# Kernel tuning notes

Measured on AMD Instinct MI355X. Metric: run time of the kernel, lower is better.

Reference implementation:

```python
import jax, jax.numpy as jnp
import numpy as np

B, S, TRG, SRC2 = 64, 2048, 512, 1024  # batch, src_len, trg_hidden, 2*src_hidden


def setup_inputs() -> dict:
    key = jax.random.key(0)
    ks = jax.random.split(key, 9)
    return {
        "dehy": jax.random.normal(ks[0], (B, TRG), dtype=jnp.float32),
        "enhy": jax.random.normal(ks[1], (B, S, SRC2), dtype=jnp.float32),
        "past_attn": jax.random.uniform(ks[2], (B, S), dtype=jnp.float32),
        "src_mask": jax.random.randint(ks[3], (B, S), 0, 2, dtype=jnp.int32),
        # parameters (torch Linear: y = x @ W.T + b)
        "W_en": jax.random.normal(ks[4], (TRG, SRC2), dtype=jnp.float32) * 0.02,
        "b_en": jnp.zeros((TRG,), dtype=jnp.float32),
        "W_de": jax.random.normal(ks[5], (TRG, TRG), dtype=jnp.float32) * 0.02,
        "w_cv": jax.random.normal(ks[6], (TRG,), dtype=jnp.float32) * 0.02,   # attn_cv_in: Linear(1, trg)
        "w_warp": jax.random.normal(ks[7], (TRG,), dtype=jnp.float32) * 0.02, # attn_warp_in: Linear(trg, 1)
    }


def reference(dehy, enhy, past_attn, src_mask, W_en, b_en, W_de, w_cv, w_warp):
    # luong_concat score with 'asee' coverage term
    # attn_agg: [B, S, TRG]
    attn_agg = (
        jnp.einsum("bsd,hd->bsh", enhy, W_en) + b_en
        + (dehy @ W_de.T)[:, None, :]
        + past_attn[..., None] * w_cv
    )
    attn_agg = jnp.tanh(attn_agg)
    attn_ee = jnp.einsum("bsh,h->bs", attn_agg, w_warp)  # [B, S]
    # masked_fill(|mask| == 0, -1e20)
    attn_ee = jnp.where(jnp.abs(src_mask) == 0, jnp.float32(-1e20), attn_ee)
    attn = jax.nn.softmax(attn_ee, axis=1)
    c_encoder = jnp.einsum("bs,bsd->bd", attn, enhy)  # [B, SRC2]
    return (c_encoder, attn, attn_ee)
```

## Files before the change

kernel.cpp:

```cpp
#include <hip/hip_runtime.h>
#include <hip/hip_bf16.h>

#define B_   64
#define S_   2048
#define TRG_ 512
#define K_   1024

typedef short short8 __attribute__((ext_vector_type(8)));
typedef short short4v __attribute__((ext_vector_type(4)));
typedef float f32x4  __attribute__((ext_vector_type(4)));
typedef unsigned short us4 __attribute__((ext_vector_type(4)));

__device__ __forceinline__ unsigned short f2bf(float f) {
    union { float f; unsigned int u; } v; v.f = f;
    unsigned int u = v.u;
    unsigned int r = (u + 0x7fffu + ((u >> 16) & 1u)) >> 16;
    return (unsigned short)r;
}

__device__ __forceinline__ short4v cvt4(f32x4 a) {
    union { __hip_bfloat162 h[2]; short4v v; } u;
    u.h[0] = __float22bfloat162_rn(float2{a[0], a[1]});
    u.h[1] = __float22bfloat162_rn(float2{a[2], a[3]});
    return u.v;
}

__global__ void wen_convert_kernel(const float* __restrict__ Wen,
                                   unsigned short* __restrict__ Wbf) {
    int idx = blockIdx.x * 256 + threadIdx.x;
    float4 f = ((const float4*)Wen)[idx];
    us4 o = { f2bf(f.x), f2bf(f.y), f2bf(f.z), f2bf(f.w) };
    ((us4*)Wbf)[idx] = o;
}

__global__ void deproj_kernel(const float* __restrict__ dehy,
                              const float* __restrict__ Wde,
                              const float* __restrict__ ben,
                              float* __restrict__ dp) {
    int b = blockIdx.x >> 1;
    int h = ((blockIdx.x & 1) << 8) + threadIdx.x;
    const float4* dv = (const float4*)(dehy + (size_t)b * TRG_);
    const float4* wv = (const float4*)(Wde + (size_t)h * TRG_);
    float s = ben[h];
    #pragma unroll 4
    for (int t = 0; t < TRG_ / 4; ++t) {
        float4 a = dv[t], w = wv[t];
        s += a.x * w.x + a.y * w.y + a.z * w.z + a.w * w.w;
    }
    dp[b * TRG_ + h] = s;
}

__global__ __launch_bounds__(512, 4) void score_kernel(
    const float* __restrict__ enhy,
    const unsigned short* __restrict__ Wbf,
    const float* __restrict__ dp,
    const float* __restrict__ past_attn,
    const int* __restrict__ src_mask,
    const float* __restrict__ w_cv,
    const float* __restrict__ w_warp,
    float* __restrict__ out_ee)
{
    __shared__ unsigned short Bbuf[2][512 * 32];
    __shared__ unsigned short Abuf[2][64 * 32];
    __shared__ float red[8][64];

    const int tid  = threadIdx.x;
    const int lane = tid & 63;
    const int w    = tid >> 6;
    const int lj   = lane & 15;
    const int lg   = lane >> 4;
    const int m0   = blockIdx.x * 64;
    const int b    = m0 >> 11;

    const int kx = ((lg ^ ((lj >> 1) & 3)) << 4);

    f32x4 acc[4][4];
    const f32x4 fz = {0.f, 0.f, 0.f, 0.f};
    #pragma unroll
    for (int i = 0; i < 4; ++i)
        #pragma unroll
        for (int j = 0; j < 4; ++j) acc[i][j] = fz;

    const int arow = tid >> 3;
    const int akq  = tid & 7;
    const float* aSrc = enhy + (size_t)(m0 + arow) * K_ + (akq << 2);
    const int aDstByte = arow * 64 + (((akq >> 1) ^ ((arow >> 1) & 3)) << 4) + ((akq & 1) << 3);

    const int brow0 = tid >> 2;
    const int bkc0  = tid & 3;
    const unsigned short* bSrc0 = Wbf + (size_t)brow0 * K_ + ((bkc0 ^ ((brow0 >> 1) & 3)) << 3);
    const int bDst0 = w * 1024;

#define LOADA(R, kt) { R = __builtin_nontemporal_load((const f32x4*)(aSrc + ((kt) << 5))); }
#define WRITEA(sel, R) { \
    *(short4v*)((char*)&Abuf[0][0] + (sel) * 4096 + aDstByte) = cvt4(R); }
#define STAGEB(sel, kt) { \
    _Pragma("unroll") \
    for (int j_ = 0; j_ < 4; ++j_) { \
        __builtin_amdgcn_global_load_lds( \
            (const __attribute__((address_space(1))) void*)(bSrc0 + (size_t)j_ * 128 * K_ + ((kt) << 5)), \
            (__attribute__((address_space(3))) void*)((char*)&Bbuf[0][0] + (sel) * 32768 + bDst0 + j_ * 8192), \
            16, 0, 0); \
    } }

    auto compute = [&](int sel) {
        const char* Bbase = (const char*)&Bbuf[0][0] + sel * 32768;
        const char* Abase = (const char*)&Abuf[0][0] + sel * 4096;
        short8 bfr[4];
        #pragma unroll
        for (int fn = 0; fn < 4; ++fn) {
            int r = (w << 6) + (fn << 4) + lj;
            bfr[fn] = *(const short8*)(Bbase + r * 64 + kx);
        }
        #pragma unroll
        for (int fm = 0; fm < 4; ++fm) {
            int rA = (fm << 4) + lj;
            short8 af = *(const short8*)(Abase + rA * 64 + kx);
            #pragma unroll
            for (int fn = 0; fn < 4; ++fn)
                acc[fm][fn] = __builtin_amdgcn_mfma_f32_16x16x32_bf16(af, bfr[fn], acc[fm][fn], 0, 0, 0);
        }
    };

    f32x4 a_c, a_n;
    LOADA(a_c, 0);
    STAGEB(0, 0);
    WRITEA(0, a_c);
    __syncthreads();

    #pragma unroll 2
    for (int kt = 0; kt < 32; ++kt) {
        const int cur = kt & 1, nxt = cur ^ 1;
        if (kt < 31) {
            STAGEB(nxt, kt + 1);
            LOADA(a_n, kt + 1);
        }
        compute(cur);
        if (kt < 31) WRITEA(nxt, a_n);
        __syncthreads();
    }

#undef LOADA
#undef WRITEA
#undef STAGEB

    float dep4[4], wcv4[4], wwp4[4];
    #pragma unroll
    for (int fn = 0; fn < 4; ++fn) {
        int h = (w << 6) + (fn << 4) + lj;
        dep4[fn] = dp[b * TRG_ + h];
        wcv4[fn] = w_cv[h];
        wwp4[fn] = w_warp[h];
    }
    #pragma unroll
    for (int fm = 0; fm < 4; ++fm) {
        #pragma unroll
        for (int reg = 0; reg < 4; ++reg) {
            int row = (fm << 4) + (lg << 2) + reg;
            float pa = past_attn[m0 + row];
            float p = 0.f;
            #pragma unroll
            for (int fn = 0; fn < 4; ++fn) {
                float v = acc[fm][fn][reg] + dep4[fn] + pa * wcv4[fn];
                float e = __expf(2.f * v);
                float t = 1.f - 2.f * __builtin_amdgcn_rcpf(e + 1.f);
                p += t * wwp4[fn];
            }
            p += __shfl_xor(p, 1);
            p += __shfl_xor(p, 2);
            p += __shfl_xor(p, 4);
            p += __shfl_xor(p, 8);
            if (lj == 0) red[w][row] = p;
        }
    }
    __syncthreads();
    if (tid < 64) {
        float ee = 0.f;
        #pragma unroll
        for (int ww = 0; ww < 8; ++ww) ee += red[ww][tid];
        int msk = src_mask[m0 + tid];
        if (msk == 0) ee = -1e20f;
        out_ee[m0 + tid] = ee;
    }
}

__global__ void softmax_kernel(const float* __restrict__ ee, float* __restrict__ attn) {
    int b = blockIdx.x, tid = threadIdx.x;
    const float* row = ee + (size_t)b * S_;
    float v[8]; float mx = -3.0e38f;
    #pragma unroll
    for (int i = 0; i < 8; ++i) { v[i] = row[tid + (i << 8)]; mx = fmaxf(mx, v[i]); }
    #pragma unroll
    for (int off = 32; off > 0; off >>= 1) mx = fmaxf(mx, __shfl_xor(mx, off));
    __shared__ float sred[4];
    int w = tid >> 6, lane = tid & 63;
    if (lane == 0) sred[w] = mx;
    __syncthreads();
    mx = fmaxf(fmaxf(sred[0], sred[1]), fmaxf(sred[2], sred[3]));
    float sum = 0.f;
    #pragma unroll
    for (int i = 0; i < 8; ++i) { v[i] = __expf(v[i] - mx); sum += v[i]; }
    #pragma unroll
    for (int off = 32; off > 0; off >>= 1) sum += __shfl_xor(sum, off);
    __syncthreads();
    if (lane == 0) sred[w] = sum;
    __syncthreads();
    sum = sred[0] + sred[1] + sred[2] + sred[3];
    float inv = 1.f / sum;
    float* orow = attn + (size_t)b * S_;
    #pragma unroll
    for (int i = 0; i < 8; ++i) orow[tid + (i << 8)] = v[i] * inv;
}

__global__ void ctx_partial_kernel(const float* __restrict__ attn,
                                   const float* __restrict__ enhy,
                                   float* __restrict__ part) {
    int bx = blockIdx.x;
    int b = bx >> 5, sc = bx & 31;
    int tid = threadIdx.x;
    const float4* e4 = (const float4*)(enhy + ((size_t)b * S_ + sc * 64) * K_);
    const float* ar = attn + (size_t)b * S_ + sc * 64;
    float4 acc = {0.f, 0.f, 0.f, 0.f};
    #pragma unroll 8
    for (int s = 0; s < 64; ++s) {
        float a = ar[s];
        float4 ev = e4[(size_t)s * 256 + tid];
        acc.x += a * ev.x; acc.y += a * ev.y; acc.z += a * ev.z; acc.w += a * ev.w;
    }
    ((float4*)part)[(size_t)(sc * 64 + b) * 256 + tid] = acc;
}

__global__ void ctx_reduce_kernel(const float* __restrict__ part, float* __restrict__ outc) {
    int idx = blockIdx.x * 256 + threadIdx.x;
    int b = idx >> 10, d = idx & 1023;
    float s = 0.f;
    #pragma unroll
    for (int sc = 0; sc < 32; ++sc) s += part[(size_t)((sc << 6) + b) * 1024 + d];
    outc[idx] = s;
}

extern "C" void kernel_launch(void* const* d_in, const int* in_sizes, int n_in,
                              void* d_out, int out_size, void* d_ws, size_t ws_size,
                              hipStream_t stream) {
    (void)in_sizes; (void)n_in; (void)out_size; (void)ws_size;

    const float* dehy = (const float*)d_in[0];
    const float* enhy = (const float*)d_in[1];
    const float* past = (const float*)d_in[2];
    const int*   mask = (const int*)d_in[3];
    const float* Wen  = (const float*)d_in[4];
    const float* ben  = (const float*)d_in[5];
    const float* Wde  = (const float*)d_in[6];
    const float* wcv  = (const float*)d_in[7];
    const float* wwp  = (const float*)d_in[8];

    float* out      = (float*)d_out;
    float* out_c    = out;
    float* out_attn = out + 65536;
    float* out_ee   = out + 65536 + 131072;

    char* ws = (char*)d_ws;
    unsigned short* Wbf = (unsigned short*)ws;
    float* dp   = (float*)(ws + (1 << 20));
    float* part = (float*)(ws + (1 << 20) + (1 << 17));

    wen_convert_kernel<<<512, 256, 0, stream>>>(Wen, Wbf);
    deproj_kernel<<<128, 256, 0, stream>>>(dehy, Wde, ben, dp);
    score_kernel<<<2048, 512, 0, stream>>>(enhy, Wbf, dp, past, mask, wcv, wwp, out_ee);
    softmax_kernel<<<64, 256, 0, stream>>>(out_ee, out_attn);
    ctx_partial_kernel<<<2048, 256, 0, stream>>>(out_attn, enhy, part);
    ctx_reduce_kernel<<<256, 256, 0, stream>>>(part, out_c);
}
```

Before: 376.8 us.

## Load W fragments directly into registers and deepen A prefetch to two stages

```diff
diff --git a/kernel.cpp b/kernel.cpp
--- a/kernel.cpp
+++ b/kernel.cpp
@@ -60,7 +60,6 @@
     const float* __restrict__ w_warp,
     float* __restrict__ out_ee)
 {
-    __shared__ unsigned short Bbuf[2][512 * 32];
     __shared__ unsigned short Abuf[2][64 * 32];
     __shared__ float red[8][64];
 
@@ -86,63 +85,56 @@
     const float* aSrc = enhy + (size_t)(m0 + arow) * K_ + (akq << 2);
     const int aDstByte = arow * 64 + (((akq >> 1) ^ ((arow >> 1) & 3)) << 4) + ((akq & 1) << 3);
 
-    const int brow0 = tid >> 2;
-    const int bkc0  = tid & 3;
-    const unsigned short* bSrc0 = Wbf + (size_t)brow0 * K_ + ((bkc0 ^ ((brow0 >> 1) & 3)) << 3);
-    const int bDst0 = w * 1024;
+    const unsigned short* bRow = Wbf + (size_t)((w << 6) + lj) * K_ + (lg << 3);
 
 #define LOADA(R, kt) { R = __builtin_nontemporal_load((const f32x4*)(aSrc + ((kt) << 5))); }
 #define WRITEA(sel, R) { \
     *(short4v*)((char*)&Abuf[0][0] + (sel) * 4096 + aDstByte) = cvt4(R); }
-#define STAGEB(sel, kt) { \
+#define LOADB(B0, B1, B2, B3, kt) { const int ko_ = (kt) << 5; \
+    B0 = *(const short8*)(bRow + (size_t)(0 * 16) * K_ + ko_); \
+    B1 = *(const short8*)(bRow + (size_t)(1 * 16) * K_ + ko_); \
+    B2 = *(const short8*)(bRow + (size_t)(2 * 16) * K_ + ko_); \
+    B3 = *(const short8*)(bRow + (size_t)(3 * 16) * K_ + ko_); }
+#define COMPUTE(sel, B0, B1, B2, B3) { \
+    const char* Abase = (const char*)&Abuf[0][0] + (sel) * 4096; \
     _Pragma("unroll") \
-    for (int j_ = 0; j_ < 4; ++j_) { \
-        __builtin_amdgcn_global_load_lds( \
-            (const __attribute__((address_space(1))) void*)(bSrc0 + (size_t)j_ * 128 * K_ + ((kt) << 5)), \
-            (__attribute__((address_space(3))) void*)((char*)&Bbuf[0][0] + (sel) * 32768 + bDst0 + j_ * 8192), \
-            16, 0, 0); \
+    for (int fm = 0; fm < 4; ++fm) { \
+        short8 af = *(const short8*)(Abase + ((fm << 4) + lj) * 64 + kx); \
+        acc[fm][0] = __builtin_amdgcn_mfma_f32_16x16x32_bf16(af, B0, acc[fm][0], 0, 0, 0); \
+        acc[fm][1] = __builtin_amdgcn_mfma_f32_16x16x32_bf16(af, B1, acc[fm][1], 0, 0, 0); \
+        acc[fm][2] = __builtin_amdgcn_mfma_f32_16x16x32_bf16(af, B2, acc[fm][2], 0, 0, 0); \
+        acc[fm][3] = __builtin_amdgcn_mfma_f32_16x16x32_bf16(af, B3, acc[fm][3], 0, 0, 0); \
     } }
 
-    auto compute = [&](int sel) {
-        const char* Bbase = (const char*)&Bbuf[0][0] + sel * 32768;
-        const char* Abase = (const char*)&Abuf[0][0] + sel * 4096;
-        short8 bfr[4];
-        #pragma unroll
-        for (int fn = 0; fn < 4; ++fn) {
-            int r = (w << 6) + (fn << 4) + lj;
-            bfr[fn] = *(const short8*)(Bbase + r * 64 + kx);
-        }
-        #pragma unroll
-        for (int fm = 0; fm < 4; ++fm) {
-            int rA = (fm << 4) + lj;
-            short8 af = *(const short8*)(Abase + rA * 64 + kx);
-            #pragma unroll
-            for (int fn = 0; fn < 4; ++fn)
-                acc[fm][fn] = __builtin_amdgcn_mfma_f32_16x16x32_bf16(af, bfr[fn], acc[fm][fn], 0, 0, 0);
-        }
-    };
-
+#define STEP(kt, BC0,BC1,BC2,BC3, BN0,BN1,BN2,BN3, AW, AL, DOB, DOA, DOW) { \
+    if (DOB) LOADB(BN0, BN1, BN2, BN3, (kt) + 1) \
+    if (DOA) LOADA(AL, (kt) + 2) \
+    COMPUTE((kt) & 1, BC0, BC1, BC2, BC3) \
+    if (DOW) WRITEA(((kt) & 1) ^ 1, AW) \
+    __syncthreads(); \
+}
+
+    short8 bA0, bA1, bA2, bA3, bB0, bB1, bB2, bB3;
     f32x4 a_c, a_n;
+
     LOADA(a_c, 0);
-    STAGEB(0, 0);
+    LOADB(bA0, bA1, bA2, bA3, 0)
     WRITEA(0, a_c);
-    __syncthreads();
-
-    #pragma unroll 2
-    for (int kt = 0; kt < 32; ++kt) {
-        const int cur = kt & 1, nxt = cur ^ 1;
-        if (kt < 31) {
-            STAGEB(nxt, kt + 1);
-            LOADA(a_n, kt + 1);
-        }
-        compute(cur);
-        if (kt < 31) WRITEA(nxt, a_n);
-        __syncthreads();
-    }
+    LOADA(a_n, 1);
+    __syncthreads();
+
+    for (int kt2 = 0; kt2 < 30; kt2 += 2) {
+        STEP(kt2,     bA0,bA1,bA2,bA3, bB0,bB1,bB2,bB3, a_n, a_c, 1, 1, 1)
+        STEP(kt2 + 1, bB0,bB1,bB2,bB3, bA0,bA1,bA2,bA3, a_c, a_n, 1, 1, 1)
+    }
+    STEP(30, bA0,bA1,bA2,bA3, bB0,bB1,bB2,bB3, a_n, a_c, 1, 0, 1)
+    STEP(31, bB0,bB1,bB2,bB3, bA0,bA1,bA2,bA3, a_c, a_n, 0, 0, 0)
 
 #undef LOADA
 #undef WRITEA
-#undef STAGEB
+#undef LOADB
+#undef COMPUTE
+#undef STEP
 
     float dep4[4], wcv4[4], wwp4[4];
     #pragma unroll
```

Result: slower. 444.4 us (+17.9%).

## Single-buffer B tile in LDS with manual waitcnt barriers and A register prefetch

Applied to the files above, without the earlier changes.

```diff
diff --git a/kernel.cpp b/kernel.cpp
--- a/kernel.cpp
+++ b/kernel.cpp
@@ -60,7 +60,7 @@
     const float* __restrict__ w_warp,
     float* __restrict__ out_ee)
 {
-    __shared__ unsigned short Bbuf[2][512 * 32];
+    __shared__ unsigned short Bbuf[512 * 32];
     __shared__ unsigned short Abuf[2][64 * 32];
     __shared__ float red[8][64];
 
@@ -94,17 +94,27 @@
 #define LOADA(R, kt) { R = __builtin_nontemporal_load((const f32x4*)(aSrc + ((kt) << 5))); }
 #define WRITEA(sel, R) { \
     *(short4v*)((char*)&Abuf[0][0] + (sel) * 4096 + aDstByte) = cvt4(R); }
-#define STAGEB(sel, kt) { \
+#define STAGEB(kt) { \
     _Pragma("unroll") \
     for (int j_ = 0; j_ < 4; ++j_) { \
         __builtin_amdgcn_global_load_lds( \
             (const __attribute__((address_space(1))) void*)(bSrc0 + (size_t)j_ * 128 * K_ + ((kt) << 5)), \
-            (__attribute__((address_space(3))) void*)((char*)&Bbuf[0][0] + (sel) * 32768 + bDst0 + j_ * 8192), \
+            (__attribute__((address_space(3))) void*)((char*)&Bbuf[0] + bDst0 + j_ * 8192), \
             16, 0, 0); \
     } }
+#define MIDBAR(N) \
+    asm volatile("s_waitcnt vmcnt(" #N ") lgkmcnt(0)" ::: "memory"); \
+    __builtin_amdgcn_sched_barrier(0); \
+    __builtin_amdgcn_s_barrier(); \
+    __builtin_amdgcn_sched_barrier(0);
+#define ENDBAR() \
+    asm volatile("s_waitcnt lgkmcnt(0)" ::: "memory"); \
+    __builtin_amdgcn_sched_barrier(0); \
+    __builtin_amdgcn_s_barrier(); \
+    __builtin_amdgcn_sched_barrier(0);
 
     auto compute = [&](int sel) {
-        const char* Bbase = (const char*)&Bbuf[0][0] + sel * 32768;
+        const char* Bbase = (const char*)&Bbuf[0];
         const char* Abase = (const char*)&Abuf[0][0] + sel * 4096;
         short8 bfr[4];
         #pragma unroll
@@ -122,27 +132,39 @@
         }
     };
 
-    f32x4 a_c, a_n;
-    LOADA(a_c, 0);
-    STAGEB(0, 0);
-    WRITEA(0, a_c);
-    __syncthreads();
-
-    #pragma unroll 2
-    for (int kt = 0; kt < 32; ++kt) {
-        const int cur = kt & 1, nxt = cur ^ 1;
-        if (kt < 31) {
-            STAGEB(nxt, kt + 1);
-            LOADA(a_n, kt + 1);
-        }
-        compute(cur);
-        if (kt < 31) WRITEA(nxt, a_n);
-        __syncthreads();
-    }
+    f32x4 aR0, aR1;
+    LOADA(aR0, 0);
+    LOADA(aR1, 1);
+    WRITEA(0, aR0);
+
+    for (int kt2 = 0; kt2 < 30; kt2 += 2) {
+        STAGEB(kt2)
+        WRITEA(1, aR1);
+        LOADA(aR0, kt2 + 2);
+        MIDBAR(1)
+        compute(0);
+        ENDBAR()
+        STAGEB(kt2 + 1)
+        WRITEA(0, aR0);
+        LOADA(aR1, kt2 + 3);
+        MIDBAR(1)
+        compute(1);
+        ENDBAR()
+    }
+    STAGEB(30)
+    WRITEA(1, aR1);
+    MIDBAR(0)
+    compute(0);
+    ENDBAR()
+    STAGEB(31)
+    MIDBAR(0)
+    compute(1);
 
 #undef LOADA
 #undef WRITEA
 #undef STAGEB
+#undef MIDBAR
+#undef ENDBAR
 
     float dep4[4], wcv4[4], wwp4[4];
     #pragma unroll
```

Result: faster. 365.0 us (-3.1%).

## Retile score GEMM to 128x128 blocks with split-H partial scores

Applied to the files above, without the earlier changes.

```diff
diff --git a/kernel.cpp b/kernel.cpp
--- a/kernel.cpp
+++ b/kernel.cpp
@@ -7,7 +7,6 @@
 #define K_   1024
 
 typedef short short8 __attribute__((ext_vector_type(8)));
-typedef short short4v __attribute__((ext_vector_type(4)));
 typedef float f32x4  __attribute__((ext_vector_type(4)));
 typedef unsigned short us4 __attribute__((ext_vector_type(4)));
 
@@ -18,10 +17,12 @@
     return (unsigned short)r;
 }
 
-__device__ __forceinline__ short4v cvt4(f32x4 a) {
-    union { __hip_bfloat162 h[2]; short4v v; } u;
+__device__ __forceinline__ short8 cvt8(f32x4 a, f32x4 b) {
+    union { __hip_bfloat162 h[4]; short8 v; } u;
     u.h[0] = __float22bfloat162_rn(float2{a[0], a[1]});
     u.h[1] = __float22bfloat162_rn(float2{a[2], a[3]});
+    u.h[2] = __float22bfloat162_rn(float2{b[0], b[1]});
+    u.h[3] = __float22bfloat162_rn(float2{b[2], b[3]});
     return u.v;
 }
 
@@ -50,26 +51,30 @@
     dp[b * TRG_ + h] = s;
 }
 
-__global__ __launch_bounds__(512, 4) void score_kernel(
+__global__ __launch_bounds__(256, 4) void score_kernel(
     const float* __restrict__ enhy,
     const unsigned short* __restrict__ Wbf,
     const float* __restrict__ dp,
     const float* __restrict__ past_attn,
-    const int* __restrict__ src_mask,
     const float* __restrict__ w_cv,
     const float* __restrict__ w_warp,
-    float* __restrict__ out_ee)
+    float* __restrict__ part_ee)
 {
-    __shared__ unsigned short Bbuf[2][512 * 32];
-    __shared__ unsigned short Abuf[2][64 * 32];
-    __shared__ float red[8][64];
+    __shared__ unsigned short Abuf[2][128 * 32];
+    __shared__ unsigned short Bbuf[2][128 * 32];
+    __shared__ float red[2][128];
 
     const int tid  = threadIdx.x;
     const int lane = tid & 63;
     const int w    = tid >> 6;
+    const int wm   = w >> 1;
+    const int wn   = w & 1;
     const int lj   = lane & 15;
     const int lg   = lane >> 4;
-    const int m0   = blockIdx.x * 64;
+    const int p    = blockIdx.x >> 2;
+    const int sl   = blockIdx.x & 3;
+    const int m0   = p << 7;
+    const int h0   = sl << 7;
     const int b    = m0 >> 11;
 
     const int kx = ((lg ^ ((lj >> 1) & 3)) << 4);
@@ -81,40 +86,45 @@
         #pragma unroll
         for (int j = 0; j < 4; ++j) acc[i][j] = fz;
 
-    const int arow = tid >> 3;
-    const int akq  = tid & 7;
-    const float* aSrc = enhy + (size_t)(m0 + arow) * K_ + (akq << 2);
-    const int aDstByte = arow * 64 + (((akq >> 1) ^ ((arow >> 1) & 3)) << 4) + ((akq & 1) << 3);
-
-    const int brow0 = tid >> 2;
-    const int bkc0  = tid & 3;
-    const unsigned short* bSrc0 = Wbf + (size_t)brow0 * K_ + ((bkc0 ^ ((brow0 >> 1) & 3)) << 3);
-    const int bDst0 = w * 1024;
-
-#define LOADA(R, kt) { R = __builtin_nontemporal_load((const f32x4*)(aSrc + ((kt) << 5))); }
-#define WRITEA(sel, R) { \
-    *(short4v*)((char*)&Abuf[0][0] + (sel) * 4096 + aDstByte) = cvt4(R); }
+    const int arow = tid >> 1;
+    const int ah   = tid & 1;
+    const float* aSrc = enhy + (size_t)(m0 + arow) * K_ + (ah << 4);
+    const int asw = (arow >> 1) & 3;
+    const int aD0 = arow * 64 + ((((ah << 1) | 0) ^ asw) << 4);
+    const int aD1 = arow * 64 + ((((ah << 1) | 1) ^ asw) << 4);
+
+    const unsigned short* bSrc0 = Wbf + (size_t)(h0 + (tid >> 2)) * K_
+                                + ((size_t)((tid & 3) ^ ((tid >> 3) & 3)) << 3);
+    const int bDst0 = (tid >> 6) << 10;
+
+#define LOADA(R0, R1, R2, R3, kt) { \
+    const float* p_ = aSrc + ((kt) << 5); \
+    R0 = *(const f32x4*)p_;       R1 = *(const f32x4*)(p_ + 4); \
+    R2 = *(const f32x4*)(p_ + 8); R3 = *(const f32x4*)(p_ + 12); }
+#define WRITEA(sel, R0, R1, R2, R3) { \
+    *(short8*)((char*)&Abuf[0][0] + (sel) * 8192 + aD0) = cvt8(R0, R1); \
+    *(short8*)((char*)&Abuf[0][0] + (sel) * 8192 + aD1) = cvt8(R2, R3); }
 #define STAGEB(sel, kt) { \
     _Pragma("unroll") \
-    for (int j_ = 0; j_ < 4; ++j_) { \
+    for (int j_ = 0; j_ < 2; ++j_) { \
         __builtin_amdgcn_global_load_lds( \
-            (const __attribute__((address_space(1))) void*)(bSrc0 + (size_t)j_ * 128 * K_ + ((kt) << 5)), \
-            (__attribute__((address_space(3))) void*)((char*)&Bbuf[0][0] + (sel) * 32768 + bDst0 + j_ * 8192), \
+            (const __attribute__((address_space(1))) void*)(bSrc0 + (size_t)j_ * 64 * K_ + ((kt) << 5)), \
+            (__attribute__((address_space(3))) void*)((char*)&Bbuf[0][0] + (sel) * 8192 + j_ * 4096 + bDst0), \
             16, 0, 0); \
     } }
 
     auto compute = [&](int sel) {
-        const char* Bbase = (const char*)&Bbuf[0][0] + sel * 32768;
-        const char* Abase = (const char*)&Abuf[0][0] + sel * 4096;
+        const char* Bbase = (const char*)&Bbuf[0][0] + sel * 8192;
+        const char* Abase = (const char*)&Abuf[0][0] + sel * 8192;
         short8 bfr[4];
         #pragma unroll
         for (int fn = 0; fn < 4; ++fn) {
-            int r = (w << 6) + (fn << 4) + lj;
+            int r = (wn << 6) + (fn << 4) + lj;
             bfr[fn] = *(const short8*)(Bbase + r * 64 + kx);
         }
         #pragma unroll
         for (int fm = 0; fm < 4; ++fm) {
-            int rA = (fm << 4) + lj;
+            int rA = (wm << 6) + (fm << 4) + lj;
             short8 af = *(const short8*)(Abase + rA * 64 + kx);
             #pragma unroll
             for (int fn = 0; fn < 4; ++fn)
@@ -122,10 +132,10 @@
         }
     };
 
-    f32x4 a_c, a_n;
-    LOADA(a_c, 0);
+    f32x4 a0, a1, a2, a3;
+    LOADA(a0, a1, a2, a3, 0);
     STAGEB(0, 0);
-    WRITEA(0, a_c);
+    WRITEA(0, a0, a1, a2, a3);
     __syncthreads();
 
     #pragma unroll 2
@@ -133,10 +143,10 @@
         const int cur = kt & 1, nxt = cur ^ 1;
         if (kt < 31) {
             STAGEB(nxt, kt + 1);
-            LOADA(a_n, kt + 1);
+            LOADA(a0, a1, a2, a3, kt + 1);
         }
         compute(cur);
-        if (kt < 31) WRITEA(nxt, a_n);
+        if (kt < 31) WRITEA(nxt, a0, a1, a2, a3);
         __syncthreads();
     }
 
@@ -147,7 +157,7 @@
     float dep4[4], wcv4[4], wwp4[4];
     #pragma unroll
     for (int fn = 0; fn < 4; ++fn) {
-        int h = (w << 6) + (fn << 4) + lj;
+        int h = h0 + (wn << 6) + (fn << 4) + lj;
         dep4[fn] = dp[b * TRG_ + h];
         wcv4[fn] = w_cv[h];
         wwp4[fn] = w_warp[h];
@@ -156,40 +166,43 @@
     for (int fm = 0; fm < 4; ++fm) {
         #pragma unroll
         for (int reg = 0; reg < 4; ++reg) {
-            int row = (fm << 4) + (lg << 2) + reg;
+            int row = (wm << 6) + (fm << 4) + (lg << 2) + reg;
             float pa = past_attn[m0 + row];
-            float p = 0.f;
+            float pp = 0.f;
             #pragma unroll
             for (int fn = 0; fn < 4; ++fn) {
                 float v = acc[fm][fn][reg] + dep4[fn] + pa * wcv4[fn];
                 float e = __expf(2.f * v);
                 float t = 1.f - 2.f * __builtin_amdgcn_rcpf(e + 1.f);
-                p += t * wwp4[fn];
+                pp += t * wwp4[fn];
             }
-            p += __shfl_xor(p, 1);
-            p += __shfl_xor(p, 2);
-            p += __shfl_xor(p, 4);
-            p += __shfl_xor(p, 8);
-            if (lj == 0) red[w][row] = p;
-        }
-    }
-    __syncthreads();
-    if (tid < 64) {
-        float ee = 0.f;
-        #pragma unroll
-        for (int ww = 0; ww < 8; ++ww) ee += red[ww][tid];
-        int msk = src_mask[m0 + tid];
-        if (msk == 0) ee = -1e20f;
-        out_ee[m0 + tid] = ee;
-    }
-}
-
-__global__ void softmax_kernel(const float* __restrict__ ee, float* __restrict__ attn) {
+            pp += __shfl_xor(pp, 1);
+            pp += __shfl_xor(pp, 2);
+            pp += __shfl_xor(pp, 4);
+            pp += __shfl_xor(pp, 8);
+            if (lj == 0) red[wn][row] = pp;
+        }
+    }
+    __syncthreads();
+    if (tid < 128)
+        part_ee[(size_t)sl * (B_ * S_) + m0 + tid] = red[0][tid] + red[1][tid];
+}
+
+__global__ void softmax_kernel(const float* __restrict__ part_ee,
+                               const int* __restrict__ src_mask,
+                               float* __restrict__ out_ee,
+                               float* __restrict__ attn) {
     int b = blockIdx.x, tid = threadIdx.x;
-    const float* row = ee + (size_t)b * S_;
     float v[8]; float mx = -3.0e38f;
     #pragma unroll
-    for (int i = 0; i < 8; ++i) { v[i] = row[tid + (i << 8)]; mx = fmaxf(mx, v[i]); }
+    for (int i = 0; i < 8; ++i) {
+        int off = b * S_ + tid + (i << 8);
+        float e = part_ee[off] + part_ee[131072 + off]
+                + part_ee[262144 + off] + part_ee[393216 + off];
+        if (src_mask[off] == 0) e = -1e20f;
+        out_ee[off] = e;
+        v[i] = e; mx = fmaxf(mx, e);
+    }
     #pragma unroll
     for (int off = 32; off > 0; off >>= 1) mx = fmaxf(mx, __shfl_xor(mx, off));
     __shared__ float sred[4];
@@ -260,14 +273,15 @@
     float* out_ee   = out + 65536 + 131072;
 
     char* ws = (char*)d_ws;
-    unsigned short* Wbf = (unsigned short*)ws;
-    float* dp   = (float*)(ws + (1 << 20));
-    float* part = (float*)(ws + (1 << 20) + (1 << 17));
+    unsigned short* Wbf  = (unsigned short*)ws;
+    float* dp      = (float*)(ws + (1 << 20));
+    float* part    = (float*)(ws + (1 << 20) + (1 << 17));
+    float* part_ee = (float*)(ws + (size_t)10 * (1 << 20));
 
     wen_convert_kernel<<<512, 256, 0, stream>>>(Wen, Wbf);
     deproj_kernel<<<128, 256, 0, stream>>>(dehy, Wde, ben, dp);
-    score_kernel<<<2048, 512, 0, stream>>>(enhy, Wbf, dp, past, mask, wcv, wwp, out_ee);
-    softmax_kernel<<<64, 256, 0, stream>>>(out_ee, out_attn);
+    score_kernel<<<4096, 256, 0, stream>>>(enhy, Wbf, dp, past, wcv, wwp, part_ee);
+    softmax_kernel<<<64, 256, 0, stream>>>(part_ee, mask, out_ee, out_attn);
     ctx_partial_kernel<<<2048, 256, 0, stream>>>(out_attn, enhy, part);
     ctx_reduce_kernel<<<256, 256, 0, stream>>>(part, out_c);
 }
```

Result: slower. 445.8 us (+18.3%).
